# Optimization experiments

Hardware: AMD Instinct MI355X
Metric: run time of the kernel (lower is better)

The kernel has to match this reference:

```python
import jax, jax.numpy as jnp
import numpy as np

BINS = 30
MOMENTUM = 0.75
LOSS_WEIGHT = 1.0


def setup_inputs() -> dict:
    key = jax.random.key(0)
    k1, k2 = jax.random.split(key)
    N, C = 8192, 2048
    preds = jax.random.normal(k1, (N, C), dtype=jnp.float32)
    targets = jax.random.randint(k2, (N, C), 0, 2).astype(jnp.int32)  # binary multi-hot
    acc_sum = jnp.zeros((BINS, C), dtype=jnp.float32)  # EMA histogram state
    return {"preds": preds, "targets": targets, "acc_sum": acc_sum}


def reference(preds, targets, acc_sum):
    N, C = preds.shape
    t = targets.astype(preds.dtype)

    # gradient norm g = |sigmoid(p) - t|, detached (weights carry no grad)
    g = jnp.abs(jax.nn.sigmoid(jax.lax.stop_gradient(preds)) - t)

    # bin index: edges[i] = i/BINS, so bin = floor(g*BINS), g=1.0 -> last bin (edge[-1]+=1e-6)
    bin_idx = jnp.clip(jnp.floor(g * BINS).astype(jnp.int32), 0, BINS - 1)  # [N, C]

    # per-label histogram: counts[b, c] = #examples with bin b in column c
    cols = jnp.broadcast_to(jnp.arange(C, dtype=jnp.int32)[None, :], (N, C))
    counts = jnp.zeros((BINS, C), dtype=preds.dtype).at[bin_idx, cols].add(1.0)

    # n[c] = number of non-empty bins for label c
    n = jnp.sum(counts >= 1.0, axis=0).astype(preds.dtype)  # [C]

    # EMA update of the histogram (momentum > 0 branch)
    acc_new = MOMENTUM * acc_sum + (1.0 - MOMENTUM) * counts  # [BINS, C]

    tot = jnp.asarray(float(max(N, 1.0)), preds.dtype)
    weights = tot / acc_new[bin_idx, cols]               # gather per-element density
    weights = weights / jnp.maximum(n, 1.0)[None, :]      # normalize by #valid bins
    weights = jax.lax.stop_gradient(weights)

    # BCE with logits, elementwise: softplus-style stable form
    bce = jnp.logaddexp(0.0, preds) - preds * t
    loss = jnp.mean(weights * bce)
    return loss * LOSS_WEIGHT
```

## Files before the change

### kernel.cpp

```cpp
#include <hip/hip_runtime.h>

#define BINS  30
#define NROWS 8192
#define NCOLS 2048
#define COLS_PER_BLK 256
#define ROWS_PER_BLK 128
#define YSLICES 64

#define FIXED_SCALE 16384.0f
#define CNT_SHIFT   24
#define SUM_MASK    ((1u << CNT_SHIFT) - 1)
#define PK_MASK     ((1u << (CNT_SHIFT + 1)) - 1)

#define WS_PART  0
#define WS_CNT   (YSLICES * BINS * NCOLS * 4)
#define WS_BSUM  (WS_CNT + BINS * NCOLS * 4)
#define WS_BPART (WS_BSUM + BINS * NCOLS * 4)
#define WS_CTR   (WS_BPART + 8 * 4)

__global__ __launch_bounds__(512, 4) void k_main(
    const float* __restrict__ preds, const int* __restrict__ targets,
    unsigned int* __restrict__ part, unsigned int* __restrict__ ctr)
{
    __shared__ __align__(16) unsigned int H[BINS * COLS_PER_BLK];
    __shared__ __align__(16) unsigned int Tb[2][8 * COLS_PER_BLK];
    const int t = threadIdx.x;
    if (blockIdx.x == 0 && blockIdx.y == 0 && t == 0) atomicExch(ctr, 0u);
    for (int i = t; i < BINS * COLS_PER_BLK; i += 512) H[i] = 0u;

    const int wrow = t >> 6;
    const int lane = t & 63;
    const int colBase = blockIdx.x * COLS_PER_BLK;
    const int col0 = colBase + 4 * lane;
    const int r0   = blockIdx.y * ROWS_PER_BLK + wrow;

    const float4* P = (const float4*)(preds   + (size_t)r0 * NCOLS + col0);
    const int4*   T = (const int4*)  (targets + (size_t)r0 * NCOLS + col0);
    const int RV8 = 8 * NCOLS / 4;

    float4 pc = P[0];
    int4   tc = T[0];
    __syncthreads();

    #pragma unroll 2
    for (int tile = 0; tile < 16; ++tile) {
        float4 pn; int4 tn;
        if (tile < 15) { P += RV8; T += RV8; pn = P[0]; tn = T[0]; }
        __builtin_amdgcn_sched_barrier(0);

        const float pv[4] = {pc.x, pc.y, pc.z, pc.w};
        const int   tv[4] = {tc.x, tc.y, tc.z, tc.w};
        unsigned int pk[4];
        #pragma unroll
        for (int j = 0; j < 4; ++j) {
            float p  = pv[j];
            float pp = tv[j] ? -p : p;
            float e  = __expf(-fabsf(pp));
            float d  = 1.0f + e;
            float r1 = __builtin_amdgcn_rcpf(d);
            float g  = (pp >= 0.0f) ? r1 : e * r1;
            int   b  = (int)(g * 30.0f);
            b = b > (BINS - 1) ? (BINS - 1) : b;
            float bce = fmaxf(pp, 0.0f) + __logf(d);
            pk[j] = ((unsigned int)b << 27) | (1u << CNT_SHIFT)
                  | (unsigned int)(bce * FIXED_SCALE + 0.5f);
        }
        uint4 w = make_uint4(pk[0], pk[1], pk[2], pk[3]);
        *((uint4*)&Tb[tile & 1][wrow * COLS_PER_BLK + 4 * lane]) = w;
        __syncthreads();

        if (t < COLS_PER_BLK) {
            unsigned int v[8];
            #pragma unroll
            for (int r = 0; r < 8; ++r)
                v[r] = Tb[tile & 1][r * COLS_PER_BLK + t];
            #pragma unroll
            for (int r = 0; r < 8; ++r) {
                const int idx = (int)(v[r] >> 27) * COLS_PER_BLK + t;
                H[idx] += v[r] & PK_MASK;
            }
        }
        if (tile < 15) { pc = pn; tc = tn; }
    }
    __syncthreads();

    const size_t outBase = (size_t)blockIdx.y * BINS * NCOLS + colBase;
    for (int i = t; i < BINS * COLS_PER_BLK; i += 512)
        part[outBase + (size_t)(i >> 8) * NCOLS + (i & 255)] = H[i];
}

__global__ __launch_bounds__(256) void k_reduce(
    const unsigned int* __restrict__ part,
    float* __restrict__ cnt_f, float* __restrict__ bsum_f)
{
    const int id = blockIdx.x * 256 + threadIdx.x;
    unsigned int cnt = 0u, sm = 0u;
    #pragma unroll 16
    for (int y = 0; y < YSLICES; ++y) {
        const unsigned int v = part[(size_t)y * BINS * NCOLS + id];
        cnt += v >> CNT_SHIFT;
        sm  += v & SUM_MASK;
    }
    cnt_f[id]  = (float)cnt;
    bsum_f[id] = (float)sm * (1.0f / FIXED_SCALE);
}

__global__ __launch_bounds__(256) void k_colsum(
    const float* __restrict__ cnt_f, const float* __restrict__ bsum_f,
    const float* __restrict__ acc_sum, float* __restrict__ blockPart,
    unsigned int* __restrict__ ctr, float* __restrict__ out)
{
    __shared__ float wave_sums[4];
    const int tid = threadIdx.x;
    const int c   = blockIdx.x * 256 + tid;

    float colsum = 0.0f;
    int n = 0;
    #pragma unroll
    for (int b = 0; b < BINS; ++b) {
        const size_t gidx = (size_t)b * NCOLS + c;
        const float cnt = cnt_f[gidx];
        if (cnt >= 1.0f) {
            n += 1;
            float acc_new = 0.75f * acc_sum[gidx] + 0.25f * cnt;
            colsum += bsum_f[gidx] / acc_new;
        }
    }
    colsum /= (float)((n > 1 ? n : 1) * NCOLS);

    #pragma unroll
    for (int off = 32; off > 0; off >>= 1)
        colsum += __shfl_down(colsum, off, 64);
    if ((tid & 63) == 0) wave_sums[tid >> 6] = colsum;
    __syncthreads();
    if (tid == 0) {
        const float s = wave_sums[0] + wave_sums[1] + wave_sums[2] + wave_sums[3];
        atomicExch(&blockPart[blockIdx.x], s);
        __threadfence();
        if (atomicAdd(ctr, 1u) == 7u) {
            __threadfence();
            double d = 0.0;
            #pragma unroll
            for (int i = 0; i < 8; ++i)
                d += (double)atomicAdd(&blockPart[i], 0.0f);
            out[0] = (float)d;
        }
    }
}

extern "C" void kernel_launch(void* const* d_in, const int* in_sizes, int n_in,
                              void* d_out, int out_size, void* d_ws, size_t ws_size,
                              hipStream_t stream)
{
    const float* preds   = (const float*)d_in[0];
    const int*   targets = (const int*)d_in[1];
    const float* acc_sum = (const float*)d_in[2];

    unsigned int* part = (unsigned int*)((char*)d_ws + WS_PART);
    float* cnt_f       = (float*)((char*)d_ws + WS_CNT);
    float* bsum_f      = (float*)((char*)d_ws + WS_BSUM);
    float* blockPart   = (float*)((char*)d_ws + WS_BPART);
    unsigned int* ctr  = (unsigned int*)((char*)d_ws + WS_CTR);

    dim3 gA(NCOLS / COLS_PER_BLK, NROWS / ROWS_PER_BLK);
    k_main<<<gA, 512, 0, stream>>>(preds, targets, part, ctr);

    k_reduce<<<(BINS * NCOLS) / 256, 256, 0, stream>>>(part, cnt_f, bsum_f);

    k_colsum<<<NCOLS / 256, 256, 0, stream>>>(cnt_f, bsum_f, acc_sum,
                                              blockPart, ctr, (float*)d_out);
}
```

Measured before the change: 183.0 us.

## Have each thread own one column and update histogram directly without staging

The main kernel now uses 256 threads, and each thread owns a single column. It loads 8 rows at a time with scalar coalesced loads and adds packed count and sum values straight into its own shared-memory histogram column. The double-buffered transpose tile and the per-tile __syncthreads are removed, and so are the bin bits packed into each value. The cost is scalar rather than float4 loads, half as many threads per block, and more elementwise work per thread, which may lower memory-level parallelism.

```diff
diff --git a/kernel.cpp b/kernel.cpp
--- a/kernel.cpp
+++ b/kernel.cpp
@@ -10,7 +10,6 @@
 #define FIXED_SCALE 16384.0f
 #define CNT_SHIFT   24
 #define SUM_MASK    ((1u << CNT_SHIFT) - 1)
-#define PK_MASK     ((1u << (CNT_SHIFT + 1)) - 1)
 
 #define WS_PART  0
 #define WS_CNT   (YSLICES * BINS * NCOLS * 4)
@@ -18,43 +17,40 @@
 #define WS_BPART (WS_BSUM + BINS * NCOLS * 4)
 #define WS_CTR   (WS_BPART + 8 * 4)
 
-__global__ __launch_bounds__(512, 4) void k_main(
+__global__ __launch_bounds__(256, 5) void k_main(
     const float* __restrict__ preds, const int* __restrict__ targets,
     unsigned int* __restrict__ part, unsigned int* __restrict__ ctr)
 {
-    __shared__ __align__(16) unsigned int H[BINS * COLS_PER_BLK];
-    __shared__ __align__(16) unsigned int Tb[2][8 * COLS_PER_BLK];
+    __shared__ unsigned int H[BINS * COLS_PER_BLK];
     const int t = threadIdx.x;
     if (blockIdx.x == 0 && blockIdx.y == 0 && t == 0) atomicExch(ctr, 0u);
-    for (int i = t; i < BINS * COLS_PER_BLK; i += 512) H[i] = 0u;
-
-    const int wrow = t >> 6;
-    const int lane = t & 63;
-    const int colBase = blockIdx.x * COLS_PER_BLK;
-    const int col0 = colBase + 4 * lane;
-    const int r0   = blockIdx.y * ROWS_PER_BLK + wrow;
-
-    const float4* P = (const float4*)(preds   + (size_t)r0 * NCOLS + col0);
-    const int4*   T = (const int4*)  (targets + (size_t)r0 * NCOLS + col0);
-    const int RV8 = 8 * NCOLS / 4;
-
-    float4 pc = P[0];
-    int4   tc = T[0];
+    #pragma unroll
+    for (int i = 0; i < BINS; ++i) H[i * COLS_PER_BLK + t] = 0u;
     __syncthreads();
 
-    #pragma unroll 2
-    for (int tile = 0; tile < 16; ++tile) {
-        float4 pn; int4 tn;
-        if (tile < 15) { P += RV8; T += RV8; pn = P[0]; tn = T[0]; }
+    const int col = blockIdx.x * COLS_PER_BLK + t;
+    const int r0  = blockIdx.y * ROWS_PER_BLK;
+    const float* P = preds   + (size_t)r0 * NCOLS + col;
+    const int*   T = targets + (size_t)r0 * NCOLS + col;
+
+    float pc[8]; int tc[8];
+    #pragma unroll
+    for (int r = 0; r < 8; ++r) { pc[r] = P[r * NCOLS]; tc[r] = T[r * NCOLS]; }
+
+    #pragma unroll 1
+    for (int batch = 0; batch < ROWS_PER_BLK / 8; ++batch) {
+        float pn[8]; int tn[8];
+        if (batch < ROWS_PER_BLK / 8 - 1) {
+            P += 8 * NCOLS; T += 8 * NCOLS;
+            #pragma unroll
+            for (int r = 0; r < 8; ++r) { pn[r] = P[r * NCOLS]; tn[r] = T[r * NCOLS]; }
+        }
         __builtin_amdgcn_sched_barrier(0);
 
-        const float pv[4] = {pc.x, pc.y, pc.z, pc.w};
-        const int   tv[4] = {tc.x, tc.y, tc.z, tc.w};
-        unsigned int pk[4];
         #pragma unroll
-        for (int j = 0; j < 4; ++j) {
-            float p  = pv[j];
-            float pp = tv[j] ? -p : p;
+        for (int r = 0; r < 8; ++r) {
+            float p  = pc[r];
+            float pp = tc[r] ? -p : p;
             float e  = __expf(-fabsf(pp));
             float d  = 1.0f + e;
             float r1 = __builtin_amdgcn_rcpf(d);
@@ -62,30 +58,18 @@
             int   b  = (int)(g * 30.0f);
             b = b > (BINS - 1) ? (BINS - 1) : b;
             float bce = fmaxf(pp, 0.0f) + __logf(d);
-            pk[j] = ((unsigned int)b << 27) | (1u << CNT_SHIFT)
-                  | (unsigned int)(bce * FIXED_SCALE + 0.5f);
+            unsigned int pk = (1u << CNT_SHIFT)
+                | (unsigned int)(bce * FIXED_SCALE + 0.5f);
+            H[b * COLS_PER_BLK + t] += pk;
         }
-        uint4 w = make_uint4(pk[0], pk[1], pk[2], pk[3]);
-        *((uint4*)&Tb[tile & 1][wrow * COLS_PER_BLK + 4 * lane]) = w;
-        __syncthreads();
-
-        if (t < COLS_PER_BLK) {
-            unsigned int v[8];
-            #pragma unroll
-            for (int r = 0; r < 8; ++r)
-                v[r] = Tb[tile & 1][r * COLS_PER_BLK + t];
-            #pragma unroll
-            for (int r = 0; r < 8; ++r) {
-                const int idx = (int)(v[r] >> 27) * COLS_PER_BLK + t;
-                H[idx] += v[r] & PK_MASK;
-            }
-        }
-        if (tile < 15) { pc = pn; tc = tn; }
+        #pragma unroll
+        for (int r = 0; r < 8; ++r) { pc[r] = pn[r]; tc[r] = tn[r]; }
     }
     __syncthreads();
 
-    const size_t outBase = (size_t)blockIdx.y * BINS * NCOLS + colBase;
-    for (int i = t; i < BINS * COLS_PER_BLK; i += 512)
+    const size_t outBase = (size_t)blockIdx.y * BINS * NCOLS
+                         + (size_t)blockIdx.x * COLS_PER_BLK;
+    for (int i = t; i < BINS * COLS_PER_BLK; i += 256)
         part[outBase + (size_t)(i >> 8) * NCOLS + (i & 255)] = H[i];
 }
 
@@ -163,7 +147,7 @@
     unsigned int* ctr  = (unsigned int*)((char*)d_ws + WS_CTR);
 
     dim3 gA(NCOLS / COLS_PER_BLK, NROWS / ROWS_PER_BLK);
-    k_main<<<gA, 512, 0, stream>>>(preds, targets, part, ctr);
+    k_main<<<gA, 256, 0, stream>>>(preds, targets, part, ctr);
 
     k_reduce<<<(BINS * NCOLS) / 256, 256, 0, stream>>>(part, cnt_f, bsum_f);
 
```

New measurement: 183.1 us. No clear change (+0.0%).
